# Performance work log

Measured on AMD Instinct MI355X. Metric: run time of the kernel, lower is better.

## Reference

```python
import jax, jax.numpy as jnp
import numpy as np

N = 100000   # num nodes
E = 20000    # num hyperedges
D = 128      # feature dim
NNZ = 600000 # incidences
EPS = 1e-5


def setup_inputs() -> dict:
    key = jax.random.key(0)
    ks = jax.random.split(key, 16)
    src = jax.random.randint(ks[0], (NNZ,), 0, N)   # node indices
    edg = jax.random.randint(ks[1], (NNZ,), 0, E)   # hyperedge indices
    edge_index = jnp.stack([src, edg]).astype(jnp.int64)
    node_attr = jax.random.normal(ks[2], (N, D), jnp.float32)
    edge_attr = jax.random.normal(ks[3], (E, D), jnp.float32)  # unused by forward
    inp = {"edge_index": edge_index, "node_attr": node_attr, "edge_attr": edge_attr}
    for l in range(3):
        inp[f"W{l+1}"] = jax.random.normal(ks[4 + l], (D, D), jnp.float32) / np.float32(np.sqrt(D))
        inp[f"b{l+1}"] = jnp.zeros((D,), jnp.float32)
        inp[f"g{l+1}"] = jnp.ones((D,), jnp.float32)
        inp[f"beta{l+1}"] = jnp.zeros((D,), jnp.float32)
    return inp


def _hconv(x, W, b, src, edg):
    # PyG HypergraphConv (no attention): out = D^{-1} H W_e B^{-1} H^T (X Theta) + b, W_e = I
    x = x @ W
    ones = jnp.ones(src.shape, x.dtype)
    deg_n = jax.ops.segment_sum(ones, src, num_segments=N)  # node degree
    deg_e = jax.ops.segment_sum(ones, edg, num_segments=E)  # hyperedge size
    Dinv = jnp.where(deg_n > 0, 1.0 / deg_n, 0.0)
    Binv = jnp.where(deg_e > 0, 1.0 / deg_e, 0.0)
    # node -> hyperedge: m_e = B^{-1} sum_{i in e} x_i
    e_feat = Binv[:, None] * jax.ops.segment_sum(x[src], edg, num_segments=E)
    # hyperedge -> node: out_i = D^{-1} sum_{e ni i} m_e
    out = Dinv[:, None] * jax.ops.segment_sum(e_feat[edg], src, num_segments=N)
    return out + b


def _bn(x, g, beta):
    # BatchNorm1d, training mode (biased variance over nodes)
    mu = jnp.mean(x, axis=0)
    var = jnp.mean((x - mu) ** 2, axis=0)
    return g * (x - mu) / jnp.sqrt(var + EPS) + beta


def reference(edge_index, node_attr, edge_attr,
              W1, b1, g1, beta1, W2, b2, g2, beta2, W3, b3, g3, beta3):
    src, edg = edge_index[0], edge_index[1]
    x = _bn(jax.nn.relu(_hconv(node_attr, W1, b1, src, edg)), g1, beta1)
    x = _bn(jax.nn.relu(_hconv(x, W2, b2, src, edg)), g2, beta2)
    x = _bn(jax.nn.relu(_hconv(x, W3, b3, src, edg)), g3, beta3)
    return x
```

## Files before the change

### kernel.cpp

```cpp
#include <hip/hip_runtime.h>
#include <stdint.h>

#define DIM 128

static inline int cdiv(long a, long b) { return (int)((a + b - 1) / b); }

typedef float f32x4 __attribute__((ext_vector_type(4)));

__device__ __forceinline__ unsigned pk_bf16(float a, float b) {
  unsigned ua = __float_as_uint(a), ub = __float_as_uint(b);
  ua = (ua + 0x7FFFu + ((ua >> 16) & 1u)) >> 16;
  ub = (ub + 0x7FFFu + ((ub >> 16) & 1u)) >> 16;
  return ua | (ub << 16);
}
__device__ __forceinline__ float bf_lo(unsigned u) { return __uint_as_float(u << 16); }
__device__ __forceinline__ float bf_hi(unsigned u) { return __uint_as_float(u & 0xFFFF0000u); }

__global__ __launch_bounds__(256) void count_kernel(
    const int* __restrict__ raw, int* __restrict__ src, int* __restrict__ edg,
    int* __restrict__ cnt, int E, int nnz) {
  bool is64;
  {
    int l = threadIdx.x & 63;
    int v = raw[2 * l + 1];
    unsigned long long m = __ballot(v == 0);
    is64 = (m == ~0ull);
  }
  int g = blockIdx.x * 256 + threadIdx.x;
  if (g < nnz) {
    int s = is64 ? raw[2 * g] : raw[g];
    int e = is64 ? raw[2 * (nnz + g)] : raw[nnz + g];
    src[g] = s;
    edg[g] = e;
    atomicAdd(&cnt[e], 1);
    atomicAdd(&cnt[E + s], 1);
  }
}

__global__ __launch_bounds__(256) void scanA_kernel(
    const int* __restrict__ cnt, int* __restrict__ P, int* __restrict__ BS, int M) {
  __shared__ int lds[256];
  int t = threadIdx.x;
  long base = blockIdx.x * 1024L;
  int v[4], ts = 0;
#pragma unroll
  for (int j = 0; j < 4; ++j) {
    long i = base + t * 4 + j;
    v[j] = (i < M) ? cnt[i] : 0;
    ts += v[j];
  }
  lds[t] = ts;
  __syncthreads();
  for (int off = 1; off < 256; off <<= 1) {
    int x = (t >= off) ? lds[t - off] : 0;
    __syncthreads();
    lds[t] += x;
    __syncthreads();
  }
  int run = lds[t] - ts;
#pragma unroll
  for (int j = 0; j < 4; ++j) {
    long i = base + t * 4 + j;
    if (i < M) P[i] = run;
    run += v[j];
  }
  if (t == 255) BS[blockIdx.x] = lds[255];
}

__global__ void scanB_kernel(int* __restrict__ BS, int* __restrict__ P,
                             int nblocks, int M) {
  if (threadIdx.x == 0) {
    int run = 0;
    for (int i = 0; i < nblocks; ++i) { int x = BS[i]; BS[i] = run; run += x; }
    P[M] = run;
  }
}

__global__ __launch_bounds__(256) void scanC_kernel(
    int* __restrict__ P, const int* __restrict__ BS, int M) {
  long i = blockIdx.x * 256L + threadIdx.x;
  if (i < M) P[i] += BS[i >> 10];
}

__global__ __launch_bounds__(256) void fill_adj_kernel(
    const int* __restrict__ src, const int* __restrict__ edg,
    const int* __restrict__ P, int* __restrict__ cnt,
    int* __restrict__ adj_e, int* __restrict__ adj_n, int E, int nnz) {
  int g = blockIdx.x * 256 + threadIdx.x;
  if (g < nnz) {
    int e = edg[g], s = src[g];
    int pe = P[e] + atomicAdd(&cnt[e], 1);
    adj_e[pe] = s;
    int pn = P[E + s] - nnz + atomicAdd(&cnt[E + s], 1);
    adj_n[pn] = e;
  }
}

__global__ void prep_w_kernel(const float* __restrict__ W,
                              const float* __restrict__ sums,
                              const float* __restrict__ sumsq,
                              const float* __restrict__ gprev,
                              const float* __restrict__ betaprev,
                              float* __restrict__ Wp, float* __restrict__ rvec,
                              int has_aff, float inv_n) {
  __shared__ float sa[DIM], sd[DIM];
  int j = threadIdx.x;
  if (has_aff) {
    float mu = sums[j] * inv_n;
    float var = fmaf(sumsq[j], inv_n, -mu * mu);
    float a = gprev[j] * rsqrtf(var + 1e-5f);
    sa[j] = a;
    sd[j] = fmaf(-mu, a, betaprev[j]);
  } else {
    sa[j] = 1.0f;
    sd[j] = 0.0f;
  }
  __syncthreads();
  float racc = 0.0f;
  for (int c = 0; c < DIM; ++c) {
    float w = W[c * DIM + j];
    Wp[c * DIM + j] = sa[c] * w;
    racc = fmaf(sd[c], w, racc);
  }
  rvec[j] = racc;
}

__global__ __launch_bounds__(256) void edge_gather_f32_kernel(
    const float4* __restrict__ X4, const int* __restrict__ P,
    const int* __restrict__ adj_e, float* __restrict__ ag, int E) {
  int slot = threadIdx.x >> 5;
  int l = threadIdx.x & 31;
  int e = blockIdx.x * 8 + slot;
  if (e >= E) return;
  int p0 = P[e], p1 = P[e + 1];
  float4 a = {0.f, 0.f, 0.f, 0.f};
  int kl = p1 - 1;
  for (int k = p0; k < p1; k += 8) {
    int n0 = adj_e[min(k, kl)];
    int n1 = adj_e[min(k + 1, kl)];
    int n2 = adj_e[min(k + 2, kl)];
    int n3 = adj_e[min(k + 3, kl)];
    int n4 = adj_e[min(k + 4, kl)];
    int n5 = adj_e[min(k + 5, kl)];
    int n6 = adj_e[min(k + 6, kl)];
    int n7 = adj_e[min(k + 7, kl)];
    float4 q0 = X4[(size_t)n0 * 32 + l];
    float4 q1 = X4[(size_t)n1 * 32 + l];
    float4 q2 = X4[(size_t)n2 * 32 + l];
    float4 q3 = X4[(size_t)n3 * 32 + l];
    float4 q4 = X4[(size_t)n4 * 32 + l];
    float4 q5 = X4[(size_t)n5 * 32 + l];
    float4 q6 = X4[(size_t)n6 * 32 + l];
    float4 q7 = X4[(size_t)n7 * 32 + l];
    a.x += ((q0.x + q1.x) + (q2.x + q3.x)) + ((q4.x + q5.x) + (q6.x + q7.x));
    a.y += ((q0.y + q1.y) + (q2.y + q3.y)) + ((q4.y + q5.y) + (q6.y + q7.y));
    a.z += ((q0.z + q1.z) + (q2.z + q3.z)) + ((q4.z + q5.z) + (q6.z + q7.z));
    a.w += ((q0.w + q1.w) + (q2.w + q3.w)) + ((q4.w + q5.w) + (q6.w + q7.w));
  }
  int deg = p1 - p0;
  if (deg > 0) {
    int extra = ((deg + 7) & ~7) - deg;
    if (extra) {
      float4 ql = X4[(size_t)adj_e[kl] * 32 + l];
      float ex = (float)extra;
      a.x -= ex * ql.x; a.y -= ex * ql.y; a.z -= ex * ql.z; a.w -= ex * ql.w;
    }
  }
  float binv = (deg > 0) ? 1.0f / (float)deg : 0.0f;
  f32x4 o;
  o.x = a.x * binv; o.y = a.y * binv; o.z = a.z * binv; o.w = a.w * binv;
  __builtin_nontemporal_store(o, &((f32x4*)ag)[(size_t)e * 32 + l]);
}

__global__ __launch_bounds__(256) void edge_gather_bf16_kernel(
    const uint2* __restrict__ xh, const int* __restrict__ P,
    const int* __restrict__ adj_e, float* __restrict__ ag, int E) {
  int slot = threadIdx.x >> 5;
  int l = threadIdx.x & 31;
  int e = blockIdx.x * 8 + slot;
  if (e >= E) return;
  int p0 = P[e], p1 = P[e + 1];
  float4 a = {0.f, 0.f, 0.f, 0.f};
  int kl = p1 - 1;
  for (int k = p0; k < p1; k += 8) {
    int n0 = adj_e[min(k, kl)];
    int n1 = adj_e[min(k + 1, kl)];
    int n2 = adj_e[min(k + 2, kl)];
    int n3 = adj_e[min(k + 3, kl)];
    int n4 = adj_e[min(k + 4, kl)];
    int n5 = adj_e[min(k + 5, kl)];
    int n6 = adj_e[min(k + 6, kl)];
    int n7 = adj_e[min(k + 7, kl)];
    uint2 q0 = xh[(size_t)n0 * 32 + l];
    uint2 q1 = xh[(size_t)n1 * 32 + l];
    uint2 q2 = xh[(size_t)n2 * 32 + l];
    uint2 q3 = xh[(size_t)n3 * 32 + l];
    uint2 q4 = xh[(size_t)n4 * 32 + l];
    uint2 q5 = xh[(size_t)n5 * 32 + l];
    uint2 q6 = xh[(size_t)n6 * 32 + l];
    uint2 q7 = xh[(size_t)n7 * 32 + l];
    a.x += ((bf_lo(q0.x) + bf_lo(q1.x)) + (bf_lo(q2.x) + bf_lo(q3.x))) +
           ((bf_lo(q4.x) + bf_lo(q5.x)) + (bf_lo(q6.x) + bf_lo(q7.x)));
    a.y += ((bf_hi(q0.x) + bf_hi(q1.x)) + (bf_hi(q2.x) + bf_hi(q3.x))) +
           ((bf_hi(q4.x) + bf_hi(q5.x)) + (bf_hi(q6.x) + bf_hi(q7.x)));
    a.z += ((bf_lo(q0.y) + bf_lo(q1.y)) + (bf_lo(q2.y) + bf_lo(q3.y))) +
           ((bf_lo(q4.y) + bf_lo(q5.y)) + (bf_lo(q6.y) + bf_lo(q7.y)));
    a.w += ((bf_hi(q0.y) + bf_hi(q1.y)) + (bf_hi(q2.y) + bf_hi(q3.y))) +
           ((bf_hi(q4.y) + bf_hi(q5.y)) + (bf_hi(q6.y) + bf_hi(q7.y)));
  }
  int deg = p1 - p0;
  if (deg > 0) {
    int extra = ((deg + 7) & ~7) - deg;
    if (extra) {
      uint2 ql = xh[(size_t)adj_e[kl] * 32 + l];
      float ex = (float)extra;
      a.x -= ex * bf_lo(ql.x); a.y -= ex * bf_hi(ql.x);
      a.z -= ex * bf_lo(ql.y); a.w -= ex * bf_hi(ql.y);
    }
  }
  float binv = (deg > 0) ? 1.0f / (float)deg : 0.0f;
  f32x4 o;
  o.x = a.x * binv; o.y = a.y * binv; o.z = a.z * binv; o.w = a.w * binv;
  __builtin_nontemporal_store(o, &((f32x4*)ag)[(size_t)e * 32 + l]);
}

__global__ __launch_bounds__(256) void gemm128_kernel(
    const float* __restrict__ X, const float* __restrict__ Wp,
    const float* __restrict__ rvec, const int* __restrict__ Pdeg,
    unsigned* __restrict__ Yh, int nrows) {
  __shared__ float sW[32 * DIM];
  __shared__ float sX[DIM * 36];
  const int t = threadIdx.x;
  const int row0 = blockIdx.x * DIM;
  const int tx = t & 15, ty = t >> 4;
  const int col0 = tx * 8, lr0 = ty * 8;
  float acc[8][8];
#pragma unroll
  for (int i = 0; i < 8; ++i)
#pragma unroll
    for (int j = 0; j < 8; ++j) acc[i][j] = 0.0f;

  for (int kc = 0; kc < 4; ++kc) {
    __syncthreads();
    {
      const float4* W4 = (const float4*)(Wp + kc * 32 * DIM);
      float4* sW4 = (float4*)sW;
#pragma unroll
      for (int i = 0; i < 4; ++i) sW4[t + i * 256] = W4[t + i * 256];
    }
#pragma unroll
    for (int i = 0; i < 4; ++i) {
      int q = t + i * 256;
      int rr = q >> 3, kq = q & 7;
      int gr = row0 + rr; if (gr >= nrows) gr = nrows - 1;
      float4 v = *(const float4*)&X[(size_t)gr * DIM + kc * 32 + kq * 4];
      *(float4*)&sX[rr * 36 + kq * 4] = v;
    }
    __syncthreads();
    for (int kk = 0; kk < 32; ++kk) {
      float4 w0 = *(const float4*)&sW[kk * DIM + col0];
      float4 w1 = *(const float4*)&sW[kk * DIM + col0 + 4];
      float wv[8] = {w0.x, w0.y, w0.z, w0.w, w1.x, w1.y, w1.z, w1.w};
      float xv[8];
#pragma unroll
      for (int i = 0; i < 8; ++i) xv[i] = sX[(lr0 + i) * 36 + kk];
#pragma unroll
      for (int i = 0; i < 8; ++i)
#pragma unroll
        for (int j = 0; j < 8; ++j) acc[i][j] = fmaf(xv[i], wv[j], acc[i][j]);
    }
  }
  float4 r0 = *(const float4*)&rvec[col0];
  float4 r1 = *(const float4*)&rvec[col0 + 4];
#pragma unroll
  for (int i = 0; i < 8; ++i) {
    int gr = row0 + lr0 + i;
    if (gr < nrows) {
      float nz = (Pdeg[gr + 1] > Pdeg[gr]) ? 1.0f : 0.0f;
      float o0x = (acc[i][0] + r0.x) * nz, o0y = (acc[i][1] + r0.y) * nz;
      float o0z = (acc[i][2] + r0.z) * nz, o0w = (acc[i][3] + r0.w) * nz;
      float o1x = (acc[i][4] + r1.x) * nz, o1y = (acc[i][5] + r1.y) * nz;
      float o1z = (acc[i][6] + r1.z) * nz, o1w = (acc[i][7] + r1.w) * nz;
      uint4 st;
      st.x = pk_bf16(o0x, o0y);
      st.y = pk_bf16(o0z, o0w);
      st.z = pk_bf16(o1x, o1y);
      st.w = pk_bf16(o1z, o1w);
      *(uint4*)&Yh[(size_t)gr * 64 + (col0 >> 1)] = st;
    }
  }
}

__global__ __launch_bounds__(256) void node_gather_kernel(
    const uint2* __restrict__ ef, const int* __restrict__ P,
    const int* __restrict__ adj_n, const float* __restrict__ b,
    uint2* __restrict__ zh, float* __restrict__ sum,
    float* __restrict__ sumsq, int E, int N, int nnz) {
  __shared__ float lsum[DIM], lsumsq[DIM];
  int t = threadIdx.x;
  if (t < DIM) { lsum[t] = 0.f; lsumsq[t] = 0.f; }
  __syncthreads();
  int slot = t >> 5;
  int l = t & 31;
  float4 bc = ((const float4*)b)[l];
  float4 s1 = {0.f, 0.f, 0.f, 0.f}, s2 = {0.f, 0.f, 0.f, 0.f};
  for (int i = blockIdx.x * 8 + slot; i < N; i += gridDim.x * 8) {
    int p0 = P[E + i] - nnz, p1 = P[E + i + 1] - nnz;
    float4 a = {0.f, 0.f, 0.f, 0.f};
    int kl = p1 - 1;
    for (int k = p0; k < p1; k += 8) {
      int e0 = adj_n[min(k, kl)];
      int e1 = adj_n[min(k + 1, kl)];
      int e2 = adj_n[min(k + 2, kl)];
      int e3 = adj_n[min(k + 3, kl)];
      int e4 = adj_n[min(k + 4, kl)];
      int e5 = adj_n[min(k + 5, kl)];
      int e6 = adj_n[min(k + 6, kl)];
      int e7 = adj_n[min(k + 7, kl)];
      uint2 q0 = ef[(size_t)e0 * 32 + l];
      uint2 q1 = ef[(size_t)e1 * 32 + l];
      uint2 q2 = ef[(size_t)e2 * 32 + l];
      uint2 q3 = ef[(size_t)e3 * 32 + l];
      uint2 q4 = ef[(size_t)e4 * 32 + l];
      uint2 q5 = ef[(size_t)e5 * 32 + l];
      uint2 q6 = ef[(size_t)e6 * 32 + l];
      uint2 q7 = ef[(size_t)e7 * 32 + l];
      a.x += ((bf_lo(q0.x) + bf_lo(q1.x)) + (bf_lo(q2.x) + bf_lo(q3.x))) +
             ((bf_lo(q4.x) + bf_lo(q5.x)) + (bf_lo(q6.x) + bf_lo(q7.x)));
      a.y += ((bf_hi(q0.x) + bf_hi(q1.x)) + (bf_hi(q2.x) + bf_hi(q3.x))) +
             ((bf_hi(q4.x) + bf_hi(q5.x)) + (bf_hi(q6.x) + bf_hi(q7.x)));
      a.z += ((bf_lo(q0.y) + bf_lo(q1.y)) + (bf_lo(q2.y) + bf_lo(q3.y))) +
             ((bf_lo(q4.y) + bf_lo(q5.y)) + (bf_lo(q6.y) + bf_lo(q7.y)));
      a.w += ((bf_hi(q0.y) + bf_hi(q1.y)) + (bf_hi(q2.y) + bf_hi(q3.y))) +
             ((bf_hi(q4.y) + bf_hi(q5.y)) + (bf_hi(q6.y) + bf_hi(q7.y)));
    }
    int deg = p1 - p0;
    if (deg > 0) {
      int extra = ((deg + 7) & ~7) - deg;
      if (extra) {
        uint2 ql = ef[(size_t)adj_n[kl] * 32 + l];
        float ex = (float)extra;
        a.x -= ex * bf_lo(ql.x); a.y -= ex * bf_hi(ql.x);
        a.z -= ex * bf_lo(ql.y); a.w -= ex * bf_hi(ql.y);
      }
    }
    float dinv = (deg > 0) ? 1.0f / (float)deg : 0.0f;
    float4 v;
    v.x = fmaxf(fmaf(dinv, a.x, bc.x), 0.f);
    v.y = fmaxf(fmaf(dinv, a.y, bc.y), 0.f);
    v.z = fmaxf(fmaf(dinv, a.z, bc.z), 0.f);
    v.w = fmaxf(fmaf(dinv, a.w, bc.w), 0.f);
    uint2 o;
    o.x = pk_bf16(v.x, v.y);
    o.y = pk_bf16(v.z, v.w);
    zh[(size_t)i * 32 + l] = o;
    s1.x += v.x; s1.y += v.y; s1.z += v.z; s1.w += v.w;
    s2.x = fmaf(v.x, v.x, s2.x); s2.y = fmaf(v.y, v.y, s2.y);
    s2.z = fmaf(v.z, v.z, s2.z); s2.w = fmaf(v.w, v.w, s2.w);
  }
  int c0 = l * 4;
  atomicAdd(&lsum[c0 + 0], s1.x); atomicAdd(&lsum[c0 + 1], s1.y);
  atomicAdd(&lsum[c0 + 2], s1.z); atomicAdd(&lsum[c0 + 3], s1.w);
  atomicAdd(&lsumsq[c0 + 0], s2.x); atomicAdd(&lsumsq[c0 + 1], s2.y);
  atomicAdd(&lsumsq[c0 + 2], s2.z); atomicAdd(&lsumsq[c0 + 3], s2.w);
  __syncthreads();
  if (t < DIM) {
    atomicAdd(&sum[t], lsum[t]);
    atomicAdd(&sumsq[t], lsumsq[t]);
  }
}

__global__ void finalize_bn_kernel(const float* __restrict__ sum,
                                   const float* __restrict__ sumsq,
                                   const float* __restrict__ g,
                                   const float* __restrict__ beta,
                                   float* __restrict__ aff_a, float* __restrict__ aff_d,
                                   int n) {
  int c = threadIdx.x;
  float inv_n = 1.0f / (float)n;
  float mu = sum[c] * inv_n;
  float var = fmaf(sumsq[c], inv_n, -mu * mu);
  float a = g[c] * rsqrtf(var + 1e-5f);
  aff_a[c] = a;
  aff_d[c] = fmaf(-mu, a, beta[c]);
}

__global__ __launch_bounds__(256) void apply_affine_kernel(
    const uint2* __restrict__ zh, const float* __restrict__ aff_a,
    const float* __restrict__ aff_d, float* __restrict__ out, long total4) {
  long i = blockIdx.x * 256L + threadIdx.x;
  if (i >= total4) return;
  int c4 = (int)(i & 31);
  float4 a = ((const float4*)aff_a)[c4];
  float4 d = ((const float4*)aff_d)[c4];
  uint2 q = zh[i];
  f32x4 o;
  o.x = fmaf(a.x, bf_lo(q.x), d.x);
  o.y = fmaf(a.y, bf_hi(q.x), d.y);
  o.z = fmaf(a.z, bf_lo(q.y), d.z);
  o.w = fmaf(a.w, bf_hi(q.y), d.w);
  __builtin_nontemporal_store(o, &((f32x4*)out)[i]);
}

extern "C" void kernel_launch(void* const* d_in, const int* in_sizes, int n_in,
                              void* d_out, int out_size, void* d_ws, size_t ws_size,
                              hipStream_t stream) {
  const int NNZv = in_sizes[0] / 2;
  const int Nv   = in_sizes[1] / DIM;
  const int Ev   = in_sizes[2] / DIM;
  const int* eidx_raw = (const int*)d_in[0];
  const float* node_attr = (const float*)d_in[1];

  float* bufE  = (float*)d_ws;
  float* Wp    = bufE + (size_t)Ev * DIM;
  float* rvec  = Wp + DIM * DIM;
  float* sums  = rvec + 128;
  float* sumsq = sums + 128;
  float* aff_a = sumsq + 128;
  float* aff_d = aff_a + 128;
  int* src   = (int*)(aff_d + 128);
  int* edg   = src + NNZv;
  int* cnt   = edg + NNZv;
  int* P     = cnt + (((size_t)Ev + Nv + 3) & ~(size_t)3);
  int* BS    = P + (((size_t)Ev + Nv + 1 + 3) & ~(size_t)3);
  int* adj_e = BS + 256;
  int* adj_n = adj_e + NNZv;
  unsigned* efh = (unsigned*)src;
  uint2* xh = (uint2*)(adj_n + NNZv);

  const int M = Ev + Nv;
  const int nbA = cdiv(M, 1024);
  const float inv_n = 1.0f / (float)Nv;

  hipMemsetAsync(cnt, 0, (size_t)M * 4, stream);
  count_kernel<<<cdiv(NNZv, 256), 256, 0, stream>>>(eidx_raw, src, edg, cnt, Ev, NNZv);
  scanA_kernel<<<nbA, 256, 0, stream>>>(cnt, P, BS, M);
  scanB_kernel<<<1, 64, 0, stream>>>(BS, P, nbA, M);
  scanC_kernel<<<cdiv(M, 256), 256, 0, stream>>>(P, BS, M);
  hipMemsetAsync(cnt, 0, (size_t)M * 4, stream);
  fill_adj_kernel<<<cdiv(NNZv, 256), 256, 0, stream>>>(src, edg, P, cnt, adj_e, adj_n, Ev, NNZv);

  for (int l = 0; l < 3; ++l) {
    const float* W     = (const float*)d_in[3 + l * 4];
    const float* b     = (const float*)d_in[4 + l * 4];
    const float* gprev    = (const float*)d_in[5 + (l > 0 ? l - 1 : 0) * 4];
    const float* betaprev = (const float*)d_in[6 + (l > 0 ? l - 1 : 0) * 4];

    prep_w_kernel<<<1, 128, 0, stream>>>(W, sums, sumsq, gprev, betaprev,
                                         Wp, rvec, l > 0 ? 1 : 0, inv_n);
    if (l == 0)
      edge_gather_f32_kernel<<<cdiv(Ev, 8), 256, 0, stream>>>(
          (const float4*)node_attr, P, adj_e, bufE, Ev);
    else
      edge_gather_bf16_kernel<<<cdiv(Ev, 8), 256, 0, stream>>>(
          xh, P, adj_e, bufE, Ev);
    gemm128_kernel<<<cdiv(Ev, DIM), 256, 0, stream>>>(bufE, Wp, rvec, P, efh, Ev);
    hipMemsetAsync(sums, 0, 256 * 4, stream);
    node_gather_kernel<<<2048, 256, 0, stream>>>(
        (const uint2*)efh, P, adj_n, b, xh, sums, sumsq, Ev, Nv, NNZv);
  }
  {
    const float* g2    = (const float*)d_in[5 + 2 * 4];
    const float* beta2 = (const float*)d_in[6 + 2 * 4];
    finalize_bn_kernel<<<1, 128, 0, stream>>>(sums, sumsq, g2, beta2, aff_a, aff_d, Nv);
  }
  apply_affine_kernel<<<cdiv((long)Nv * 32, 256), 256, 0, stream>>>(
      xh, aff_a, aff_d, (float*)d_out, (long)Nv * 32);
}
```

Before: 714.4 us.

## Parallelize weight prep, deepen edge gather unroll, interleave two nodes per warp in node gather

```diff
diff --git a/kernel.cpp b/kernel.cpp
--- a/kernel.cpp
+++ b/kernel.cpp
@@ -15,6 +15,17 @@
 }
 __device__ __forceinline__ float bf_lo(unsigned u) { return __uint_as_float(u << 16); }
 __device__ __forceinline__ float bf_hi(unsigned u) { return __uint_as_float(u & 0xFFFF0000u); }
+
+__device__ __forceinline__ void acc8(float4& a, const uint2* q) {
+  a.x += ((bf_lo(q[0].x) + bf_lo(q[1].x)) + (bf_lo(q[2].x) + bf_lo(q[3].x))) +
+         ((bf_lo(q[4].x) + bf_lo(q[5].x)) + (bf_lo(q[6].x) + bf_lo(q[7].x)));
+  a.y += ((bf_hi(q[0].x) + bf_hi(q[1].x)) + (bf_hi(q[2].x) + bf_hi(q[3].x))) +
+         ((bf_hi(q[4].x) + bf_hi(q[5].x)) + (bf_hi(q[6].x) + bf_hi(q[7].x)));
+  a.z += ((bf_lo(q[0].y) + bf_lo(q[1].y)) + (bf_lo(q[2].y) + bf_lo(q[3].y))) +
+         ((bf_lo(q[4].y) + bf_lo(q[5].y)) + (bf_lo(q[6].y) + bf_lo(q[7].y)));
+  a.w += ((bf_hi(q[0].y) + bf_hi(q[1].y)) + (bf_hi(q[2].y) + bf_hi(q[3].y))) +
+         ((bf_hi(q[4].y) + bf_hi(q[5].y)) + (bf_hi(q[6].y) + bf_hi(q[7].y)));
+}
 
 __global__ __launch_bounds__(256) void count_kernel(
     const int* __restrict__ raw, int* __restrict__ src, int* __restrict__ edg,
@@ -96,33 +107,34 @@
   }
 }
 
-__global__ void prep_w_kernel(const float* __restrict__ W,
-                              const float* __restrict__ sums,
-                              const float* __restrict__ sumsq,
-                              const float* __restrict__ gprev,
-                              const float* __restrict__ betaprev,
-                              float* __restrict__ Wp, float* __restrict__ rvec,
-                              int has_aff, float inv_n) {
-  __shared__ float sa[DIM], sd[DIM];
-  int j = threadIdx.x;
-  if (has_aff) {
-    float mu = sums[j] * inv_n;
-    float var = fmaf(sumsq[j], inv_n, -mu * mu);
-    float a = gprev[j] * rsqrtf(var + 1e-5f);
-    sa[j] = a;
-    sd[j] = fmaf(-mu, a, betaprev[j]);
-  } else {
-    sa[j] = 1.0f;
-    sd[j] = 0.0f;
-  }
+__global__ __launch_bounds__(256) void prep_w_kernel(
+    const float* __restrict__ W, const float* __restrict__ sums,
+    const float* __restrict__ sumsq, const float* __restrict__ gprev,
+    const float* __restrict__ betaprev, float* __restrict__ Wp,
+    float* __restrict__ rvec, int has_aff, float inv_n) {
+  __shared__ float red[256];
+  int t = threadIdx.x;
+  int j = t & 127;
+  int half = t >> 7;
+  int c0 = blockIdx.x * 16 + half * 8;
+  float racc = 0.f;
+#pragma unroll
+  for (int cc = 0; cc < 8; ++cc) {
+    int c = c0 + cc;
+    float a = 1.0f, d = 0.0f;
+    if (has_aff) {
+      float mu = sums[c] * inv_n;
+      float var = fmaf(sumsq[c], inv_n, -mu * mu);
+      a = gprev[c] * rsqrtf(var + 1e-5f);
+      d = fmaf(-mu, a, betaprev[c]);
+    }
+    float w = W[c * DIM + j];
+    Wp[c * DIM + j] = a * w;
+    racc = fmaf(d, w, racc);
+  }
+  red[t] = racc;
   __syncthreads();
-  float racc = 0.0f;
-  for (int c = 0; c < DIM; ++c) {
-    float w = W[c * DIM + j];
-    Wp[c * DIM + j] = sa[c] * w;
-    racc = fmaf(sd[c], w, racc);
-  }
-  rvec[j] = racc;
+  if (t < 128) atomicAdd(&rvec[j], red[t] + red[t + 128]);
 }
 
 __global__ __launch_bounds__(256) void edge_gather_f32_kernel(
@@ -182,35 +194,19 @@
   int p0 = P[e], p1 = P[e + 1];
   float4 a = {0.f, 0.f, 0.f, 0.f};
   int kl = p1 - 1;
-  for (int k = p0; k < p1; k += 8) {
-    int n0 = adj_e[min(k, kl)];
-    int n1 = adj_e[min(k + 1, kl)];
-    int n2 = adj_e[min(k + 2, kl)];
-    int n3 = adj_e[min(k + 3, kl)];
-    int n4 = adj_e[min(k + 4, kl)];
-    int n5 = adj_e[min(k + 5, kl)];
-    int n6 = adj_e[min(k + 6, kl)];
-    int n7 = adj_e[min(k + 7, kl)];
-    uint2 q0 = xh[(size_t)n0 * 32 + l];
-    uint2 q1 = xh[(size_t)n1 * 32 + l];
-    uint2 q2 = xh[(size_t)n2 * 32 + l];
-    uint2 q3 = xh[(size_t)n3 * 32 + l];
-    uint2 q4 = xh[(size_t)n4 * 32 + l];
-    uint2 q5 = xh[(size_t)n5 * 32 + l];
-    uint2 q6 = xh[(size_t)n6 * 32 + l];
-    uint2 q7 = xh[(size_t)n7 * 32 + l];
-    a.x += ((bf_lo(q0.x) + bf_lo(q1.x)) + (bf_lo(q2.x) + bf_lo(q3.x))) +
-           ((bf_lo(q4.x) + bf_lo(q5.x)) + (bf_lo(q6.x) + bf_lo(q7.x)));
-    a.y += ((bf_hi(q0.x) + bf_hi(q1.x)) + (bf_hi(q2.x) + bf_hi(q3.x))) +
-           ((bf_hi(q4.x) + bf_hi(q5.x)) + (bf_hi(q6.x) + bf_hi(q7.x)));
-    a.z += ((bf_lo(q0.y) + bf_lo(q1.y)) + (bf_lo(q2.y) + bf_lo(q3.y))) +
-           ((bf_lo(q4.y) + bf_lo(q5.y)) + (bf_lo(q6.y) + bf_lo(q7.y)));
-    a.w += ((bf_hi(q0.y) + bf_hi(q1.y)) + (bf_hi(q2.y) + bf_hi(q3.y))) +
-           ((bf_hi(q4.y) + bf_hi(q5.y)) + (bf_hi(q6.y) + bf_hi(q7.y)));
+  for (int k = p0; k < p1; k += 16) {
+    int n[16];
+#pragma unroll
+    for (int j = 0; j < 16; ++j) n[j] = adj_e[min(k + j, kl)];
+    uint2 q[16];
+#pragma unroll
+    for (int j = 0; j < 16; ++j) q[j] = xh[(size_t)n[j] * 32 + l];
+    acc8(a, q);
+    acc8(a, q + 8);
   }
   int deg = p1 - p0;
   if (deg > 0) {
-    int extra = ((deg + 7) & ~7) - deg;
+    int extra = ((deg + 15) & ~15) - deg;
     if (extra) {
       uint2 ql = xh[(size_t)adj_e[kl] * 32 + l];
       float ex = (float)extra;
@@ -304,59 +300,89 @@
   int l = t & 31;
   float4 bc = ((const float4*)b)[l];
   float4 s1 = {0.f, 0.f, 0.f, 0.f}, s2 = {0.f, 0.f, 0.f, 0.f};
-  for (int i = blockIdx.x * 8 + slot; i < N; i += gridDim.x * 8) {
-    int p0 = P[E + i] - nnz, p1 = P[E + i + 1] - nnz;
-    float4 a = {0.f, 0.f, 0.f, 0.f};
-    int kl = p1 - 1;
-    for (int k = p0; k < p1; k += 8) {
-      int e0 = adj_n[min(k, kl)];
-      int e1 = adj_n[min(k + 1, kl)];
-      int e2 = adj_n[min(k + 2, kl)];
-      int e3 = adj_n[min(k + 3, kl)];
-      int e4 = adj_n[min(k + 4, kl)];
-      int e5 = adj_n[min(k + 5, kl)];
-      int e6 = adj_n[min(k + 6, kl)];
-      int e7 = adj_n[min(k + 7, kl)];
-      uint2 q0 = ef[(size_t)e0 * 32 + l];
-      uint2 q1 = ef[(size_t)e1 * 32 + l];
-      uint2 q2 = ef[(size_t)e2 * 32 + l];
-      uint2 q3 = ef[(size_t)e3 * 32 + l];
-      uint2 q4 = ef[(size_t)e4 * 32 + l];
-      uint2 q5 = ef[(size_t)e5 * 32 + l];
-      uint2 q6 = ef[(size_t)e6 * 32 + l];
-      uint2 q7 = ef[(size_t)e7 * 32 + l];
-      a.x += ((bf_lo(q0.x) + bf_lo(q1.x)) + (bf_lo(q2.x) + bf_lo(q3.x))) +
-             ((bf_lo(q4.x) + bf_lo(q5.x)) + (bf_lo(q6.x) + bf_lo(q7.x)));
-      a.y += ((bf_hi(q0.x) + bf_hi(q1.x)) + (bf_hi(q2.x) + bf_hi(q3.x))) +
-             ((bf_hi(q4.x) + bf_hi(q5.x)) + (bf_hi(q6.x) + bf_hi(q7.x)));
-      a.z += ((bf_lo(q0.y) + bf_lo(q1.y)) + (bf_lo(q2.y) + bf_lo(q3.y))) +
-             ((bf_lo(q4.y) + bf_lo(q5.y)) + (bf_lo(q6.y) + bf_lo(q7.y)));
-      a.w += ((bf_hi(q0.y) + bf_hi(q1.y)) + (bf_hi(q2.y) + bf_hi(q3.y))) +
-             ((bf_hi(q4.y) + bf_hi(q5.y)) + (bf_hi(q6.y) + bf_hi(q7.y)));
-    }
-    int deg = p1 - p0;
-    if (deg > 0) {
-      int extra = ((deg + 7) & ~7) - deg;
-      if (extra) {
-        uint2 ql = ef[(size_t)adj_n[kl] * 32 + l];
-        float ex = (float)extra;
-        a.x -= ex * bf_lo(ql.x); a.y -= ex * bf_hi(ql.x);
-        a.z -= ex * bf_lo(ql.y); a.w -= ex * bf_hi(ql.y);
-      }
-    }
-    float dinv = (deg > 0) ? 1.0f / (float)deg : 0.0f;
-    float4 v;
-    v.x = fmaxf(fmaf(dinv, a.x, bc.x), 0.f);
-    v.y = fmaxf(fmaf(dinv, a.y, bc.y), 0.f);
-    v.z = fmaxf(fmaf(dinv, a.z, bc.z), 0.f);
-    v.w = fmaxf(fmaf(dinv, a.w, bc.w), 0.f);
-    uint2 o;
-    o.x = pk_bf16(v.x, v.y);
-    o.y = pk_bf16(v.z, v.w);
-    zh[(size_t)i * 32 + l] = o;
-    s1.x += v.x; s1.y += v.y; s1.z += v.z; s1.w += v.w;
-    s2.x = fmaf(v.x, v.x, s2.x); s2.y = fmaf(v.y, v.y, s2.y);
-    s2.z = fmaf(v.z, v.z, s2.z); s2.w = fmaf(v.w, v.w, s2.w);
+  const int G = gridDim.x * 8;
+  for (int i = blockIdx.x * 8 + slot; i < N; i += 2 * G) {
+    int iB = i + G;
+    bool hasB = iB < N;
+    int pA0 = P[E + i] - nnz, pA1 = P[E + i + 1] - nnz;
+    int pB0 = 0, pB1 = 0;
+    if (hasB) { pB0 = P[E + iB] - nnz; pB1 = P[E + iB + 1] - nnz; }
+    float4 aA = {0.f, 0.f, 0.f, 0.f}, aB = {0.f, 0.f, 0.f, 0.f};
+    int klA = pA1 - 1, klB = pB1 - 1;
+    int kA = pA0, kB = pB0;
+    while ((kA < pA1) || (kB < pB1)) {
+      bool dA = kA < pA1, dB = kB < pB1;
+      int eA[8], eB[8];
+      if (dA) {
+#pragma unroll
+        for (int j = 0; j < 8; ++j) eA[j] = adj_n[min(kA + j, klA)];
+      }
+      if (dB) {
+#pragma unroll
+        for (int j = 0; j < 8; ++j) eB[j] = adj_n[min(kB + j, klB)];
+      }
+      uint2 qA[8], qB[8];
+      if (dA) {
+#pragma unroll
+        for (int j = 0; j < 8; ++j) qA[j] = ef[(size_t)eA[j] * 32 + l];
+      }
+      if (dB) {
+#pragma unroll
+        for (int j = 0; j < 8; ++j) qB[j] = ef[(size_t)eB[j] * 32 + l];
+      }
+      if (dA) { acc8(aA, qA); kA += 8; }
+      if (dB) { acc8(aB, qB); kB += 8; }
+    }
+    {
+      int deg = pA1 - pA0;
+      if (deg > 0) {
+        int extra = ((deg + 7) & ~7) - deg;
+        if (extra) {
+          uint2 ql = ef[(size_t)adj_n[klA] * 32 + l];
+          float ex = (float)extra;
+          aA.x -= ex * bf_lo(ql.x); aA.y -= ex * bf_hi(ql.x);
+          aA.z -= ex * bf_lo(ql.y); aA.w -= ex * bf_hi(ql.y);
+        }
+      }
+      float dinv = (deg > 0) ? 1.0f / (float)deg : 0.0f;
+      float4 v;
+      v.x = fmaxf(fmaf(dinv, aA.x, bc.x), 0.f);
+      v.y = fmaxf(fmaf(dinv, aA.y, bc.y), 0.f);
+      v.z = fmaxf(fmaf(dinv, aA.z, bc.z), 0.f);
+      v.w = fmaxf(fmaf(dinv, aA.w, bc.w), 0.f);
+      uint2 o;
+      o.x = pk_bf16(v.x, v.y);
+      o.y = pk_bf16(v.z, v.w);
+      zh[(size_t)i * 32 + l] = o;
+      s1.x += v.x; s1.y += v.y; s1.z += v.z; s1.w += v.w;
+      s2.x = fmaf(v.x, v.x, s2.x); s2.y = fmaf(v.y, v.y, s2.y);
+      s2.z = fmaf(v.z, v.z, s2.z); s2.w = fmaf(v.w, v.w, s2.w);
+    }
+    if (hasB) {
+      int deg = pB1 - pB0;
+      if (deg > 0) {
+        int extra = ((deg + 7) & ~7) - deg;
+        if (extra) {
+          uint2 ql = ef[(size_t)adj_n[klB] * 32 + l];
+          float ex = (float)extra;
+          aB.x -= ex * bf_lo(ql.x); aB.y -= ex * bf_hi(ql.x);
+          aB.z -= ex * bf_lo(ql.y); aB.w -= ex * bf_hi(ql.y);
+        }
+      }
+      float dinv = (deg > 0) ? 1.0f / (float)deg : 0.0f;
+      float4 v;
+      v.x = fmaxf(fmaf(dinv, aB.x, bc.x), 0.f);
+      v.y = fmaxf(fmaf(dinv, aB.y, bc.y), 0.f);
+      v.z = fmaxf(fmaf(dinv, aB.z, bc.z), 0.f);
+      v.w = fmaxf(fmaf(dinv, aB.w, bc.w), 0.f);
+      uint2 o;
+      o.x = pk_bf16(v.x, v.y);
+      o.y = pk_bf16(v.z, v.w);
+      zh[(size_t)iB * 32 + l] = o;
+      s1.x += v.x; s1.y += v.y; s1.z += v.z; s1.w += v.w;
+      s2.x = fmaf(v.x, v.x, s2.x); s2.y = fmaf(v.y, v.y, s2.y);
+      s2.z = fmaf(v.z, v.z, s2.z); s2.w = fmaf(v.w, v.w, s2.w);
+    }
   }
   int c0 = l * 4;
   atomicAdd(&lsum[c0 + 0], s1.x); atomicAdd(&lsum[c0 + 1], s1.y);
@@ -446,7 +472,8 @@
     const float* gprev    = (const float*)d_in[5 + (l > 0 ? l - 1 : 0) * 4];
     const float* betaprev = (const float*)d_in[6 + (l > 0 ? l - 1 : 0) * 4];
 
-    prep_w_kernel<<<1, 128, 0, stream>>>(W, sums, sumsq, gprev, betaprev,
+    hipMemsetAsync(rvec, 0, 128 * 4, stream);
+    prep_w_kernel<<<8, 256, 0, stream>>>(W, sums, sumsq, gprev, betaprev,
                                          Wp, rvec, l > 0 ? 1 : 0, inv_n);
     if (l == 0)
       edge_gather_f32_kernel<<<cdiv(Ev, 8), 256, 0, stream>>>(
```

After: 702.9 us. No clear change (-1.6%).
